# Kernel optimization log

Hardware: AMD Instinct MI355X
Metric: run time of the kernel (lower is better)

Reference implementation:

```python
import jax, jax.numpy as jnp
import numpy as np


def _nn_shift(x, dr):
    # Nearest-neighbor per-batch integer shift with edge clamping, matching
    # fcn_nn_spl: pad by 1, shift clipped indices, slice interior, gather.
    xp = jnp.pad(x, ((0, 0), (1, 1), (1, 1), (0, 0)))
    B, ny, nx, _ = xp.shape
    d = jnp.round(dr).astype(jnp.int32)            # [B,2] = (dx, dy)
    ix = jnp.clip(jnp.arange(nx, dtype=jnp.int32)[None, :] + d[:, 0:1], 0, nx - 1)[:, 1:-1]  # [B,W]
    iy = jnp.clip(jnp.arange(ny, dtype=jnp.int32)[None, :] + d[:, 1:2], 0, ny - 1)[:, 1:-1]  # [B,H]
    gather_one = lambda xb, iyb, ixb: xb[iyb][:, ixb]  # [H+2,W+2,C] -> [H,W,C]
    return jax.vmap(gather_one)(xp, iy, ix)


def setup_inputs() -> dict:
    key = jax.random.key(0)
    k1, k2 = jax.random.split(key)
    x = jax.random.normal(k1, (32, 512, 512, 4), dtype=jnp.float32)
    mk = jax.random.uniform(k2, (32, 512, 512, 1), dtype=jnp.float32)
    return {"x": x, "mk": mk}


def reference(x, mk):
    B, H, W, _ = mk.shape
    # mask moments -> centroid offset per batch element
    m00 = jnp.maximum(0.001, jnp.sum(mk, axis=(1, 2, 3)))              # [B]
    ry = (jnp.arange(H, dtype=jnp.float32) - (H // 2)).reshape(1, H, 1, 1)
    rx = (jnp.arange(W, dtype=jnp.float32) - (W // 2)).reshape(1, 1, W, 1)
    m10 = jnp.sum(rx * mk, axis=(1, 2, 3))                             # [B]
    m01 = jnp.sum(ry * mk, axis=(1, 2, 3))                             # [B]
    dr = jnp.stack([m10 / m00, m01 / m00], axis=1)                     # [B,2] (dx,dy)
    return _nn_shift(x, dr)
```

## Files before the change

### kernel.cpp

```cpp
#include <hip/hip_runtime.h>
#include <hip/hip_bf16.h>


#define RB 32
#define NB 32
#define HPIX 512
#define WPIX 512
#define PIX_PER_BATCH (HPIX * WPIX)

__global__ __launch_bounds__(256) void moments_kernel(const float* __restrict__ mk,
                                                      float* __restrict__ partials) {
    const int b   = blockIdx.x / RB;
    const int blk = blockIdx.x % RB;
    const int tid = threadIdx.x;

    const float4* mk4 = (const float4*)(mk + (size_t)b * PIX_PER_BATCH);
    float a0 = 0.f, ax = 0.f, ay = 0.f;
    const int base = blk * 2048 + tid;
#pragma unroll
    for (int it = 0; it < 8; ++it) {
        const int q = base + it * 256;
        const float4 v = mk4[q];
        const int p  = q << 2;
        const int y  = p >> 9;
        const int x0 = p & 511;
        const float wy = (float)(y - 256);
        const float s  = v.x + v.y + v.z + v.w;
        a0 += s;
        ay += wy * s;
        ax += (float)(x0 - 256) * v.x + (float)(x0 - 255) * v.y +
              (float)(x0 - 254) * v.z + (float)(x0 - 253) * v.w;
    }
    __shared__ float r0[256], rx[256], ry[256];
    r0[tid] = a0; rx[tid] = ax; ry[tid] = ay;
    __syncthreads();
    for (int s = 128; s > 0; s >>= 1) {
        if (tid < s) {
            r0[tid] += r0[tid + s];
            rx[tid] += rx[tid + s];
            ry[tid] += ry[tid + s];
        }
        __syncthreads();
    }
    if (tid == 0) {
        float* pb = partials + (size_t)(b * RB + blk) * 3;
        pb[0] = r0[0]; pb[1] = rx[0]; pb[2] = ry[0];
    }
}

__global__ void finalize_kernel(const float* __restrict__ partials,
                                int2* __restrict__ d) {
    const int b = threadIdx.x;
    if (b < NB) {
        float s0 = 0.f, sx = 0.f, sy = 0.f;
        for (int i = 0; i < RB; ++i) {
            const float* p = partials + (size_t)(b * RB + i) * 3;
            s0 += p[0]; sx += p[1]; sy += p[2];
        }
        const float m00 = fmaxf(0.001f, s0);
        d[b] = make_int2((int)rintf(sx / m00), (int)rintf(sy / m00));
    }
}

__global__ __launch_bounds__(256) void shift_kernel(const float4* __restrict__ x,
                                                    const int2* __restrict__ d,
                                                    float4* __restrict__ out) {
    const int gid = blockIdx.x * 256 + threadIdx.x;
    const int b  = gid >> 18;
    const int ij = gid & (PIX_PER_BATCH - 1);
    const int i  = ij >> 9;
    const int j  = ij & 511;
    const int2 db = d[b];
    const int sx = j + db.x;
    const int sy = i + db.y;
    float4 v = make_float4(0.f, 0.f, 0.f, 0.f);
    if ((unsigned)sx < (unsigned)WPIX && (unsigned)sy < (unsigned)HPIX) {
        v = x[((size_t)b << 18) + (sy << 9) + sx];
    }
    out[gid] = v;
}

extern "C" void kernel_launch(void* const* d_in, const int* in_sizes, int n_in,
                              void* d_out, int out_size, void* d_ws, size_t ws_size,
                              hipStream_t stream) {
    const float* x  = (const float*)d_in[0];
    const float* mk = (const float*)d_in[1];
    float* out = (float*)d_out;

    float* partials = (float*)d_ws;
    int2*  d        = (int2*)((char*)d_ws + (size_t)3 * NB * RB * sizeof(float));

    moments_kernel<<<NB * RB, 256, 0, stream>>>(mk, partials);
    finalize_kernel<<<1, 64, 0, stream>>>(partials, d);
    shift_kernel<<<(NB * PIX_PER_BATCH) / 256, 256, 0, stream>>>(
        (const float4*)x, d, (float4*)out);
}
```

Baseline: 246.6 us.

## Fuse finalize into shift kernel, process 4 pixels per thread, nontemporal stores

Drops the separate single-block finalize launch. Each shift block now reduces its batch's 32 partial moments in shared memory to get the integer shift. Each thread also handles four pixels instead of one, and output is written with nontemporal stores so it does not pollute the cache. This removes one kernel launch and its serialization gap. The cost is that every block redoes a tiny reduction and waits on two barriers.

Measured after the change: 255.2 us. 3.5% more time.

```diff
diff --git a/kernel.cpp b/kernel.cpp
--- a/kernel.cpp
+++ b/kernel.cpp
@@ -1,5 +1,4 @@
 #include <hip/hip_runtime.h>
-#include <hip/hip_bf16.h>
 
 
 #define RB 32
@@ -7,6 +6,10 @@
 #define HPIX 512
 #define WPIX 512
 #define PIX_PER_BATCH (HPIX * WPIX)
+#define PPT 4
+#define PIX_PER_BLOCK (256 * PPT)
+
+typedef float f32x4 __attribute__((ext_vector_type(4)));
 
 __global__ __launch_bounds__(256) void moments_kernel(const float* __restrict__ mk,
                                                       float* __restrict__ partials) {
@@ -48,36 +51,43 @@
     }
 }
 
-__global__ void finalize_kernel(const float* __restrict__ partials,
-                                int2* __restrict__ d) {
-    const int b = threadIdx.x;
-    if (b < NB) {
+__global__ __launch_bounds__(256) void shift_kernel(const f32x4* __restrict__ x,
+                                                    const float* __restrict__ partials,
+                                                    f32x4* __restrict__ out) {
+    const int tid  = threadIdx.x;
+    const int pix0 = blockIdx.x * PIX_PER_BLOCK;
+    const int b    = pix0 >> 18;
+
+    __shared__ float sp[RB * 3];
+    __shared__ int2  sd;
+    if (tid < RB * 3) sp[tid] = partials[(size_t)b * RB * 3 + tid];
+    __syncthreads();
+    if (tid == 0) {
         float s0 = 0.f, sx = 0.f, sy = 0.f;
         for (int i = 0; i < RB; ++i) {
-            const float* p = partials + (size_t)(b * RB + i) * 3;
-            s0 += p[0]; sx += p[1]; sy += p[2];
+            s0 += sp[3 * i]; sx += sp[3 * i + 1]; sy += sp[3 * i + 2];
         }
         const float m00 = fmaxf(0.001f, s0);
-        d[b] = make_int2((int)rintf(sx / m00), (int)rintf(sy / m00));
+        sd = make_int2((int)rintf(sx / m00), (int)rintf(sy / m00));
     }
-}
+    __syncthreads();
+    const int2 db = sd;
+    const size_t xbase = (size_t)b << 18;
 
-__global__ __launch_bounds__(256) void shift_kernel(const float4* __restrict__ x,
-                                                    const int2* __restrict__ d,
-                                                    float4* __restrict__ out) {
-    const int gid = blockIdx.x * 256 + threadIdx.x;
-    const int b  = gid >> 18;
-    const int ij = gid & (PIX_PER_BATCH - 1);
-    const int i  = ij >> 9;
-    const int j  = ij & 511;
-    const int2 db = d[b];
-    const int sx = j + db.x;
-    const int sy = i + db.y;
-    float4 v = make_float4(0.f, 0.f, 0.f, 0.f);
-    if ((unsigned)sx < (unsigned)WPIX && (unsigned)sy < (unsigned)HPIX) {
-        v = x[((size_t)b << 18) + (sy << 9) + sx];
+    int idx = pix0 + tid;
+#pragma unroll
+    for (int k = 0; k < PPT; ++k, idx += 256) {
+        const int ij = idx & (PIX_PER_BATCH - 1);
+        const int i  = ij >> 9;
+        const int j  = ij & 511;
+        const int sxp = j + db.x;
+        const int syp = i + db.y;
+        f32x4 v = (f32x4)0.f;
+        if ((unsigned)sxp < (unsigned)WPIX && (unsigned)syp < (unsigned)HPIX) {
+            v = x[xbase + ((size_t)syp << 9) + sxp];
+        }
+        __builtin_nontemporal_store(v, &out[idx]);
     }
-    out[gid] = v;
 }
 
 extern "C" void kernel_launch(void* const* d_in, const int* in_sizes, int n_in,
@@ -88,10 +98,8 @@
     float* out = (float*)d_out;
 
     float* partials = (float*)d_ws;
-    int2*  d        = (int2*)((char*)d_ws + (size_t)3 * NB * RB * sizeof(float));
 
     moments_kernel<<<NB * RB, 256, 0, stream>>>(mk, partials);
-    finalize_kernel<<<1, 64, 0, stream>>>(partials, d);
-    shift_kernel<<<(NB * PIX_PER_BATCH) / 256, 256, 0, stream>>>(
-        (const float4*)x, d, (float4*)out);
+    shift_kernel<<<(NB * PIX_PER_BATCH) / PIX_PER_BLOCK, 256, 0, stream>>>(
+        (const f32x4*)x, partials, (f32x4*)out);
 }
```

## Rewrite shift kernel as persistent blocks with batched clamped loads

Applied to the files above, without the earlier changes.

Replaces the one-pixel-per-thread shift kernel with 512 persistent blocks. Each thread loops over its chunk and issues 8 unconditional loads per iteration, using clamped indices so every load is in bounds, before a scheduling barrier and the masked stores. The aim is more memory-level parallelism and fewer launched blocks for this bandwidth-bound copy. In exchange it uses more registers per thread and leaves only 512 blocks to fill the GPU.

New measurement: 258.5 us. +4.8%, slower.

```diff
diff --git a/kernel.cpp b/kernel.cpp
--- a/kernel.cpp
+++ b/kernel.cpp
@@ -1,5 +1,4 @@
 #include <hip/hip_runtime.h>
-#include <hip/hip_bf16.h>
 
 
 #define RB 32
@@ -7,6 +6,16 @@
 #define HPIX 512
 #define WPIX 512
 #define PIX_PER_BATCH (HPIX * WPIX)
+#define TOTAL_PIX (NB * PIX_PER_BATCH)
+
+#define SBLOCKS 512
+#define STHREADS 256
+#define PIX_PER_SBLOCK (TOTAL_PIX / SBLOCKS)
+#define SBLK_PER_BATCH (PIX_PER_BATCH / PIX_PER_SBLOCK)
+#define BATCH 8
+#define SITERS (PIX_PER_SBLOCK / (BATCH * STHREADS))
+
+typedef float f32x4 __attribute__((ext_vector_type(4)));
 
 __global__ __launch_bounds__(256) void moments_kernel(const float* __restrict__ mk,
                                                       float* __restrict__ partials) {
@@ -62,22 +71,40 @@
     }
 }
 
-__global__ __launch_bounds__(256) void shift_kernel(const float4* __restrict__ x,
-                                                    const int2* __restrict__ d,
-                                                    float4* __restrict__ out) {
-    const int gid = blockIdx.x * 256 + threadIdx.x;
-    const int b  = gid >> 18;
-    const int ij = gid & (PIX_PER_BATCH - 1);
-    const int i  = ij >> 9;
-    const int j  = ij & 511;
+__global__ __launch_bounds__(256, 2) void shift_kernel(const f32x4* __restrict__ x,
+                                                       const int2* __restrict__ d,
+                                                       f32x4* __restrict__ out) {
+    const int tid = threadIdx.x;
+    const int blk = blockIdx.x;
+    const int b   = blk >> 4;
     const int2 db = d[b];
-    const int sx = j + db.x;
-    const int sy = i + db.y;
-    float4 v = make_float4(0.f, 0.f, 0.f, 0.f);
-    if ((unsigned)sx < (unsigned)WPIX && (unsigned)sy < (unsigned)HPIX) {
-        v = x[((size_t)b << 18) + (sy << 9) + sx];
+    const int base = (blk & (SBLK_PER_BATCH - 1)) * PIX_PER_SBLOCK;
+    const f32x4* __restrict__ xb = x + ((size_t)b << 18);
+    f32x4* __restrict__ ob = out + ((size_t)b << 18) + base;
+
+#pragma unroll 1
+    for (int it = 0; it < SITERS; ++it) {
+        f32x4 v[BATCH];
+        bool  ok[BATCH];
+#pragma unroll
+        for (int j = 0; j < BATCH; ++j) {
+            const int ij  = base + it * (BATCH * STHREADS) + j * STHREADS + tid;
+            const int row = ij >> 9;
+            const int col = ij & 511;
+            const int sx  = col + db.x;
+            const int sy  = row + db.y;
+            ok[j] = ((unsigned)sx < (unsigned)WPIX) && ((unsigned)sy < (unsigned)HPIX);
+            const int cx = min(max(sx, 0), WPIX - 1);
+            const int cy = min(max(sy, 0), HPIX - 1);
+            v[j] = xb[(cy << 9) | cx];
+        }
+        __builtin_amdgcn_sched_barrier(0);
+#pragma unroll
+        for (int j = 0; j < BATCH; ++j) {
+            if (!ok[j]) v[j] = (f32x4)0.f;
+            ob[it * (BATCH * STHREADS) + j * STHREADS + tid] = v[j];
+        }
     }
-    out[gid] = v;
 }
 
 extern "C" void kernel_launch(void* const* d_in, const int* in_sizes, int n_in,
@@ -92,6 +119,6 @@
 
     moments_kernel<<<NB * RB, 256, 0, stream>>>(mk, partials);
     finalize_kernel<<<1, 64, 0, stream>>>(partials, d);
-    shift_kernel<<<(NB * PIX_PER_BATCH) / 256, 256, 0, stream>>>(
-        (const float4*)x, d, (float4*)out);
+    shift_kernel<<<SBLOCKS, STHREADS, 0, stream>>>(
+        (const f32x4*)x, d, (f32x4*)out);
 }
```

## Copy input with device memcpy and fix up only shifted batches

Applied to the files above, without the earlier changes.

Replaces the per-pixel gather kernel with a device-to-device copy of the whole input into the output, followed by a fixup kernel. Each fixup block returns early when its batch's rounded shift is zero, and otherwise rewrites its pixels with the shifted, zero-filled gather, four pixels per thread. The aim is to let the runtime's copy path move the bulk of the data when shifts are small. In exchange it adds an extra launch, and any batch with a nonzero shift is written twice.

Result: slower. 272.8 us (+10.6%).

```diff
diff --git a/kernel.cpp b/kernel.cpp
--- a/kernel.cpp
+++ b/kernel.cpp
@@ -1,5 +1,4 @@
 #include <hip/hip_runtime.h>
-#include <hip/hip_bf16.h>
 
 
 #define RB 32
@@ -7,6 +6,15 @@
 #define HPIX 512
 #define WPIX 512
 #define PIX_PER_BATCH (HPIX * WPIX)
+#define TOTAL_PIX (NB * PIX_PER_BATCH)
+#define X_BYTES ((size_t)TOTAL_PIX * 16)
+
+#define FPPT 4
+#define FIX_THREADS 256
+#define PIX_PER_FBLOCK (FIX_THREADS * FPPT)
+#define FIX_BLOCKS (TOTAL_PIX / PIX_PER_FBLOCK)
+
+typedef float f32x4 __attribute__((ext_vector_type(4)));
 
 __global__ __launch_bounds__(256) void moments_kernel(const float* __restrict__ mk,
                                                       float* __restrict__ partials) {
@@ -62,22 +70,30 @@
     }
 }
 
-__global__ __launch_bounds__(256) void shift_kernel(const float4* __restrict__ x,
+__global__ __launch_bounds__(256) void fixup_kernel(const f32x4* __restrict__ x,
                                                     const int2* __restrict__ d,
-                                                    float4* __restrict__ out) {
-    const int gid = blockIdx.x * 256 + threadIdx.x;
-    const int b  = gid >> 18;
-    const int ij = gid & (PIX_PER_BATCH - 1);
-    const int i  = ij >> 9;
-    const int j  = ij & 511;
-    const int2 db = d[b];
-    const int sx = j + db.x;
-    const int sy = i + db.y;
-    float4 v = make_float4(0.f, 0.f, 0.f, 0.f);
-    if ((unsigned)sx < (unsigned)WPIX && (unsigned)sy < (unsigned)HPIX) {
-        v = x[((size_t)b << 18) + (sy << 9) + sx];
+                                                    f32x4* __restrict__ out) {
+    const int pix0 = blockIdx.x * PIX_PER_FBLOCK;
+    const int b    = pix0 >> 18;
+    const int2 db  = d[b];
+    if ((db.x | db.y) == 0) return;
+
+    const int tid = threadIdx.x;
+    const f32x4* __restrict__ xb = x + ((size_t)b << 18);
+    int idx = pix0 + tid;
+#pragma unroll
+    for (int k = 0; k < FPPT; ++k, idx += FIX_THREADS) {
+        const int ij = idx & (PIX_PER_BATCH - 1);
+        const int i  = ij >> 9;
+        const int j  = ij & 511;
+        const int sx = j + db.x;
+        const int sy = i + db.y;
+        f32x4 v = (f32x4)0.f;
+        if ((unsigned)sx < (unsigned)WPIX && (unsigned)sy < (unsigned)HPIX) {
+            v = xb[(sy << 9) + sx];
+        }
+        out[idx] = v;
     }
-    out[gid] = v;
 }
 
 extern "C" void kernel_launch(void* const* d_in, const int* in_sizes, int n_in,
@@ -92,6 +108,7 @@
 
     moments_kernel<<<NB * RB, 256, 0, stream>>>(mk, partials);
     finalize_kernel<<<1, 64, 0, stream>>>(partials, d);
-    shift_kernel<<<(NB * PIX_PER_BATCH) / 256, 256, 0, stream>>>(
-        (const float4*)x, d, (float4*)out);
+    hipMemcpyAsync(out, x, X_BYTES, hipMemcpyDeviceToDevice, stream);
+    fixup_kernel<<<FIX_BLOCKS, FIX_THREADS, 0, stream>>>(
+        (const f32x4*)x, d, (f32x4*)out);
 }
```
